# Performance work log

Measured on AMD Instinct MI355X. Metric: run time of the kernel, lower is better.

Reference implementation:

```python
import jax, jax.numpy as jnp
import numpy as np

N = 2048      # nodes: 8 sequences x 256 tokens
E = 524288    # edges: dense attention graph, 8 * 256^2
H = 8         # heads
DK = 64       # per-head dim


def setup_inputs() -> dict:
    key = jax.random.key(0)
    k1, k2, k3, k4, k5 = jax.random.split(key, 5)
    q = jax.random.normal(k1, (N, H, DK), dtype=jnp.float32)
    k = jax.random.normal(k2, (N, H, DK), dtype=jnp.float32)
    v = jax.random.normal(k3, (N, H, DK), dtype=jnp.float32)
    edge_src = jax.random.randint(k4, (E,), 0, N, dtype=jnp.int32)
    edge_dst = jax.random.randint(k5, (E,), 0, N, dtype=jnp.int32)
    return {"q": q, "k": k, "v": v, "edge_src": edge_src, "edge_dst": edge_dst}


def reference(q, k, v, edge_src, edge_dst):
    # src_dot_dst('k','q','score'): per-edge dot product over head dim -> [E, H]
    score = jnp.einsum('ehd,ehd->eh', k[edge_src], q[edge_dst])
    # scaled_exp('score', sqrt(d_k)): exp(clamp(score / sqrt(d_k), -10, 10))
    score = jnp.exp(jnp.clip(score / jnp.sqrt(jnp.float32(DK)), -10.0, 10.0))
    # send_and_recv: wv = sum_dst(v_src * score), z = sum_dst(score)
    wv = jax.ops.segment_sum(v[edge_src] * score[:, :, None], edge_dst, num_segments=N)  # [N, H, DK]
    z = jax.ops.segment_sum(score, edge_dst, num_segments=N)  # [N, H]
    # post_func normalization: attention output per node
    return wv / z[:, :, None]
```

## Files before the change

kernel.cpp:

```cpp
#include <hip/hip_runtime.h>

#define NNODES 2048
#define NHEAD 8
#define DKDIM 64

typedef unsigned int uint;
typedef unsigned short ushort;
typedef unsigned char uchar;
typedef __fp16 h2 __attribute__((ext_vector_type(2)));
typedef __fp16 h8 __attribute__((ext_vector_type(8)));
typedef float f4 __attribute__((ext_vector_type(4)));

#define KSCALE 0.18033688011112042f
#define CLAMP2 14.426950408889634f

__device__ __forceinline__ uint pk2(float a, float b) {
    union { h2 h; uint u; } x; x.h = __builtin_amdgcn_cvt_pkrtz(a, b); return x.u;
}

__global__ void conv_k(const float* __restrict__ k, uint4* __restrict__ kc,
                       uint4* __restrict__ A4) {
    int i = blockIdx.x * 256 + threadIdx.x;
    int dim8 = i & 7, node = (i >> 3) & 2047, h = i >> 14;
    const float* src = k + (size_t)node * 512 + h * 64 + dim8 * 8;
    float4 f0 = *(const float4*)src;
    float4 f1 = *(const float4*)(src + 4);
    uint4 o;
    o.x = pk2(f0.x * KSCALE, f0.y * KSCALE);
    o.y = pk2(f0.z * KSCALE, f0.w * KSCALE);
    o.z = pk2(f1.x * KSCALE, f1.y * KSCALE);
    o.w = pk2(f1.z * KSCALE, f1.w * KSCALE);
    kc[(h * 2048 + node) * 8 + dim8] = o;
    uint4 zz = {0u, 0u, 0u, 0u};
    A4[i] = zz;
    A4[i + 131072] = zz;
}

__global__ void conv_vT(const float* __restrict__ v, ushort* __restrict__ vt) {
    __shared__ float tile[64][65];
    int b = blockIdx.x;
    int h = b & 7, tn = b >> 3;
    int t = threadIdx.x;
    int nl = t >> 2, dq = (t & 3) * 16;
    const float* src = v + ((size_t)(tn * 64 + nl)) * 512 + h * 64 + dq;
#pragma unroll
    for (int i = 0; i < 4; ++i) {
        float4 f = *(const float4*)(src + i * 4);
        tile[nl][dq + i * 4 + 0] = f.x;
        tile[nl][dq + i * 4 + 1] = f.y;
        tile[nl][dq + i * 4 + 2] = f.z;
        tile[nl][dq + i * 4 + 3] = f.w;
    }
    __syncthreads();
    int dim = t >> 2, nq = (t & 3) * 16;
    uint wv[8];
#pragma unroll
    for (int i = 0; i < 8; ++i)
        wv[i] = pk2(tile[nq + 2 * i][dim], tile[nq + 2 * i + 1][dim]);
    char* base = (char*)vt + ((size_t)(h * 64 + dim) * 2048 + tn * 64) * 2;
    int nb0 = (t & 3) * 2;
    uint4 lo = { wv[0], wv[1], wv[2], wv[3] };
    uint4 hi = { wv[4], wv[5], wv[6], wv[7] };
    *(uint4*)(base + nb0 * 16) = lo;
    *(uint4*)(base + nb0 * 16 + 16) = hi;
}

__global__ void histA(const int* __restrict__ es, const int* __restrict__ ed,
                      uint* __restrict__ A32, int E) {
    int i = blockIdx.x * 256 + threadIdx.x;
    if (i < E) {
        uint idx = (uint)es[i] * 2048u + (uint)ed[i];
        atomicAdd(&A32[idx >> 2], 1u << ((idx & 3) * 8));
    }
}

__global__ void __launch_bounds__(512, 1) attn_kernel(
    const float* __restrict__ q, const ushort* __restrict__ kc, const ushort* __restrict__ vt,
    const uchar* __restrict__ A8, float* __restrict__ out) {
    __shared__ __align__(16) char LK[2][2][8192];
    __shared__ __align__(16) char LV[2][2][8192];
    __shared__ __align__(16) char LA[2][2][4096];
    __shared__ __align__(16) char LS[8][2304];

    int b = blockIdx.x;
    int h = b & 7;
    int dst0 = (b >> 3) * 64;
    int t = threadIdx.x;
    int w = t >> 6, half = w >> 2, wq = w & 3;
    int l = t & 63, c = l & 15, g = l >> 4;
    int ht = t & 255;

    const char* kH = (const char*)kc + (size_t)h * 262144;
    const char* vH = (const char*)vt + (size_t)h * 262144;

    h8 qf[2];
    {
        const float* qp = q + (size_t)(dst0 + wq * 16 + c) * 512 + h * 64 + g * 8;
#pragma unroll
        for (int ch = 0; ch < 2; ++ch) {
            float4 f0 = *(const float4*)(qp + ch * 32);
            float4 f1 = *(const float4*)(qp + ch * 32 + 4);
            union { uint u[4]; h8 v; } U;
            U.u[0] = pk2(f0.x, f0.y); U.u[1] = pk2(f0.z, f0.w);
            U.u[2] = pk2(f1.x, f1.y); U.u[3] = pk2(f1.z, f1.w);
            qf[ch] = U.v;
        }
    }

    f4 of[4];
#pragma unroll
    for (int i = 0; i < 4; ++i) of[i] = (f4){0.f, 0.f, 0.f, 0.f};
    float z = 0.f;

    int r0 = ht >> 3, b0 = ht & 7;
    int ar_ = ht >> 2, as_ = ht & 3;
    uint4 kr[2], vr[2], ar;
    int ts0 = half * 16;

#pragma unroll
    for (int j = 0; j < 2; ++j) {
        int row = r0 + j * 32;
        kr[j] = *(const uint4*)(kH + (size_t)(ts0 * 64 + row) * 128 + b0 * 16);
        vr[j] = *(const uint4*)(vH + (size_t)row * 4096 + ts0 * 128 + b0 * 16);
        *(uint4*)(LK[half][0] + row * 128 + b0 * 16) = kr[j];
        *(uint4*)(LV[half][0] + row * 128 + b0 * 16) = vr[j];
    }
    ar = *(const uint4*)(A8 + (size_t)(ts0 * 64 + ar_) * 2048 + dst0 + as_ * 16);
    *(uint4*)(LA[half][0] + ar_ * 64 + as_ * 16) = ar;
    __syncthreads();

    for (int it = 0; it < 16; ++it) {
        int cur = it & 1;
        int ts = ts0 + it;
        if (it < 15) {
#pragma unroll
            for (int j = 0; j < 2; ++j) {
                int row = r0 + j * 32;
                kr[j] = *(const uint4*)(kH + (size_t)((ts + 1) * 64 + row) * 128 + b0 * 16);
                vr[j] = *(const uint4*)(vH + (size_t)row * 4096 + (ts + 1) * 128 + b0 * 16);
            }
            ar = *(const uint4*)(A8 + (size_t)((ts + 1) * 64 + ar_) * 2048 + dst0 + as_ * 16);
        }

        f4 sacc[4];
#pragma unroll
        for (int i = 0; i < 4; ++i) sacc[i] = (f4){0.f, 0.f, 0.f, 0.f};
#pragma unroll
        for (int nt = 0; nt < 4; ++nt)
#pragma unroll
            for (int ch = 0; ch < 2; ++ch) {
                h8 kf = *(const h8*)(LK[half][cur] + (nt * 16 + c) * 128 + (ch * 4 + g) * 16);
                sacc[nt] = __builtin_amdgcn_mfma_f32_16x16x32_f16(kf, qf[ch], sacc[nt], 0, 0, 0);
            }

        char* Sw = LS[w];
        const uchar* Ac = (const uchar*)LA[half][cur];
#pragma unroll
        for (int nt = 0; nt < 4; ++nt)
#pragma unroll
            for (int r = 0; r < 4; ++r) {
                float sc = fminf(fmaxf(sacc[nt][r], -CLAMP2), CLAMP2);
                float m = (float)Ac[(nt * 16 + 4 * g + r) * 64 + wq * 16 + c];
                float e = exp2f(sc) * m;
                z += e;
                *(ushort*)(Sw + c * 144 + (nt * 16 + 4 * g + r) * 2) = (ushort)pk2(e, e);
            }
        asm volatile("" ::: "memory");

        h8 sf[2];
#pragma unroll
        for (int ch = 0; ch < 2; ++ch)
            sf[ch] = *(const h8*)(Sw + c * 144 + (ch * 32 + 8 * g) * 2);
#pragma unroll
        for (int nt = 0; nt < 4; ++nt)
#pragma unroll
            for (int ch = 0; ch < 2; ++ch) {
                h8 vf = *(const h8*)(LV[half][cur] + (nt * 16 + c) * 128 + (ch * 4 + g) * 16);
                of[nt] = __builtin_amdgcn_mfma_f32_16x16x32_f16(vf, sf[ch], of[nt], 0, 0, 0);
            }

        if (it < 15) {
            int nb = cur ^ 1;
#pragma unroll
            for (int j = 0; j < 2; ++j) {
                int row = r0 + j * 32;
                *(uint4*)(LK[half][nb] + row * 128 + b0 * 16) = kr[j];
                *(uint4*)(LV[half][nb] + row * 128 + b0 * 16) = vr[j];
            }
            *(uint4*)(LA[half][nb] + ar_ * 64 + as_ * 16) = ar;
        }
        __syncthreads();
    }

    z += __shfl_xor(z, 16);
    z += __shfl_xor(z, 32);

    float* CL = (float*)&LK[0][0][0];
    float* CLz = (float*)&LV[0][0][0];
    if (half == 1) {
#pragma unroll
        for (int nt = 0; nt < 4; ++nt)
#pragma unroll
            for (int r = 0; r < 4; ++r)
                CL[(wq * 16 + c) * 65 + nt * 16 + 4 * g + r] = of[nt][r];
        if (l < 16) CLz[wq * 16 + c] = z;
    }
    __syncthreads();
    if (half == 0) {
        float zt = 1.0f / (z + CLz[wq * 16 + c]);
#pragma unroll
        for (int nt = 0; nt < 4; ++nt)
#pragma unroll
            for (int r = 0; r < 4; ++r) {
                int idx = (wq * 16 + c) * 65 + nt * 16 + 4 * g + r;
                CL[idx] = (of[nt][r] + CL[idx]) * zt;
            }
    }
    __syncthreads();
#pragma unroll
    for (int j = 0; j < 8; ++j) {
        int i2 = w * 8 + j;
        out[(size_t)(dst0 + i2) * 512 + h * 64 + l] = CL[i2 * 65 + l];
    }
}


extern "C" void kernel_launch(void* const* d_in, const int* in_sizes, int n_in,
                              void* d_out, int out_size, void* d_ws, size_t ws_size,
                              hipStream_t stream) {
    const float* q = (const float*)d_in[0];
    const float* k = (const float*)d_in[1];
    const float* v = (const float*)d_in[2];
    const int* esrc = (const int*)d_in[3];
    const int* edst = (const int*)d_in[4];
    float* out = (float*)d_out;
    const int E = in_sizes[3];

    uchar* A8 = (uchar*)d_ws;
    ushort* kc = (ushort*)(A8 + (size_t)NNODES * NNODES);
    ushort* vt = kc + (size_t)NHEAD * NNODES * DKDIM;

    conv_k<<<512, 256, 0, stream>>>(k, (uint4*)kc, (uint4*)A8);
    conv_vT<<<256, 256, 0, stream>>>(v, vt);
    histA<<<(E + 255) / 256, 256, 0, stream>>>(esrc, edst, (uint*)A8, E);
    attn_kernel<<<256, 512, 0, stream>>>(q, kc, vt, A8, out);
}
```

Before: 69.28 us.

## Merge vT and histogram kernels, swizzle LDS, shuffle scores, transpose adjacency

Merges the V-transpose and edge-histogram prep kernels into one launch, which removes a kernel launch. Stores the adjacency count matrix as [dst][src] so each lane reads its four counts with a single 32-bit LDS load. Applies an XOR swizzle to the K/V LDS tiles to reduce bank conflicts, and passes the exp scores to the second MFMA through cross-lane shuffles instead of an LDS scratch round-trip. Adds s_setprio around the MFMA blocks; the shuffle-based transpose adds ALU and select work in exchange for less LDS traffic.

```diff
diff --git a/kernel.cpp b/kernel.cpp
--- a/kernel.cpp
+++ b/kernel.cpp
@@ -18,8 +18,8 @@
     union { h2 h; uint u; } x; x.h = __builtin_amdgcn_cvt_pkrtz(a, b); return x.u;
 }
 
-__global__ void conv_k(const float* __restrict__ k, uint4* __restrict__ kc,
-                       uint4* __restrict__ A4) {
+__global__ void prep1(const float* __restrict__ k, uint4* __restrict__ kc,
+                      uint4* __restrict__ A4) {
     int i = blockIdx.x * 256 + threadIdx.x;
     int dim8 = i & 7, node = (i >> 3) & 2047, h = i >> 14;
     const float* src = k + (size_t)node * 512 + h * 64 + dim8 * 8;
@@ -36,41 +36,42 @@
     A4[i + 131072] = zz;
 }
 
-__global__ void conv_vT(const float* __restrict__ v, ushort* __restrict__ vt) {
+__global__ void prep2(const float* __restrict__ v, ushort* __restrict__ vt,
+                      const int* __restrict__ es, const int* __restrict__ ed,
+                      uint* __restrict__ A32, int E) {
     __shared__ float tile[64][65];
     int b = blockIdx.x;
-    int h = b & 7, tn = b >> 3;
     int t = threadIdx.x;
-    int nl = t >> 2, dq = (t & 3) * 16;
-    const float* src = v + ((size_t)(tn * 64 + nl)) * 512 + h * 64 + dq;
-#pragma unroll
-    for (int i = 0; i < 4; ++i) {
-        float4 f = *(const float4*)(src + i * 4);
-        tile[nl][dq + i * 4 + 0] = f.x;
-        tile[nl][dq + i * 4 + 1] = f.y;
-        tile[nl][dq + i * 4 + 2] = f.z;
-        tile[nl][dq + i * 4 + 3] = f.w;
-    }
-    __syncthreads();
-    int dim = t >> 2, nq = (t & 3) * 16;
-    uint wv[8];
-#pragma unroll
-    for (int i = 0; i < 8; ++i)
-        wv[i] = pk2(tile[nq + 2 * i][dim], tile[nq + 2 * i + 1][dim]);
-    char* base = (char*)vt + ((size_t)(h * 64 + dim) * 2048 + tn * 64) * 2;
-    int nb0 = (t & 3) * 2;
-    uint4 lo = { wv[0], wv[1], wv[2], wv[3] };
-    uint4 hi = { wv[4], wv[5], wv[6], wv[7] };
-    *(uint4*)(base + nb0 * 16) = lo;
-    *(uint4*)(base + nb0 * 16 + 16) = hi;
-}
-
-__global__ void histA(const int* __restrict__ es, const int* __restrict__ ed,
-                      uint* __restrict__ A32, int E) {
-    int i = blockIdx.x * 256 + threadIdx.x;
-    if (i < E) {
-        uint idx = (uint)es[i] * 2048u + (uint)ed[i];
-        atomicAdd(&A32[idx >> 2], 1u << ((idx & 3) * 8));
+    if (b < 256) {
+        int h = b & 7, tn = b >> 3;
+        int nl = t >> 2, dq = (t & 3) * 16;
+        const float* src = v + ((size_t)(tn * 64 + nl)) * 512 + h * 64 + dq;
+#pragma unroll
+        for (int i = 0; i < 4; ++i) {
+            float4 f = *(const float4*)(src + i * 4);
+            tile[nl][dq + i * 4 + 0] = f.x;
+            tile[nl][dq + i * 4 + 1] = f.y;
+            tile[nl][dq + i * 4 + 2] = f.z;
+            tile[nl][dq + i * 4 + 3] = f.w;
+        }
+        __syncthreads();
+        int dim = t >> 2, nq = (t & 3) * 16;
+        uint wv[8];
+#pragma unroll
+        for (int i = 0; i < 8; ++i)
+            wv[i] = pk2(tile[nq + 2 * i][dim], tile[nq + 2 * i + 1][dim]);
+        char* base = (char*)vt + ((size_t)(b & 7) * 64 + dim) * 4096 + (b >> 3) * 128;
+        int nb0 = (t & 3) * 2;
+        uint4 lo = { wv[0], wv[1], wv[2], wv[3] };
+        uint4 hi = { wv[4], wv[5], wv[6], wv[7] };
+        *(uint4*)(base + nb0 * 16) = lo;
+        *(uint4*)(base + nb0 * 16 + 16) = hi;
+    } else {
+        int i = (b - 256) * 256 + t;
+        if (i < E) {
+            uint idx = (uint)ed[i] * 2048u + (uint)es[i];
+            atomicAdd(&A32[idx >> 2], 1u << ((idx & 3) * 8));
+        }
     }
 }
 
@@ -79,8 +80,7 @@
     const uchar* __restrict__ A8, float* __restrict__ out) {
     __shared__ __align__(16) char LK[2][2][8192];
     __shared__ __align__(16) char LV[2][2][8192];
-    __shared__ __align__(16) char LA[2][2][4096];
-    __shared__ __align__(16) char LS[8][2304];
+    __shared__ __align__(16) char LA[2][2][5120];
 
     int b = blockIdx.x;
     int h = b & 7;
@@ -114,20 +114,23 @@
 
     int r0 = ht >> 3, b0 = ht & 7;
     int ar_ = ht >> 2, as_ = ht & 3;
+    int ts0 = half * 16;
     uint4 kr[2], vr[2], ar;
-    int ts0 = half * 16;
 
 #pragma unroll
     for (int j = 0; j < 2; ++j) {
         int row = r0 + j * 32;
         kr[j] = *(const uint4*)(kH + (size_t)(ts0 * 64 + row) * 128 + b0 * 16);
         vr[j] = *(const uint4*)(vH + (size_t)row * 4096 + ts0 * 128 + b0 * 16);
-        *(uint4*)(LK[half][0] + row * 128 + b0 * 16) = kr[j];
-        *(uint4*)(LV[half][0] + row * 128 + b0 * 16) = vr[j];
-    }
-    ar = *(const uint4*)(A8 + (size_t)(ts0 * 64 + ar_) * 2048 + dst0 + as_ * 16);
-    *(uint4*)(LA[half][0] + ar_ * 64 + as_ * 16) = ar;
+        *(uint4*)(LK[half][0] + row * 128 + (b0 ^ (row & 7)) * 16) = kr[j];
+        *(uint4*)(LV[half][0] + row * 128 + (b0 ^ (row & 7)) * 16) = vr[j];
+    }
+    ar = *(const uint4*)(A8 + (size_t)(dst0 + ar_) * 2048 + ts0 * 64 + as_ * 16);
+    *(uint4*)(LA[half][0] + ar_ * 80 + as_ * 16) = ar;
     __syncthreads();
+
+    int sl = c + 32 * (g & 1);
+    bool hi = (g >> 1) != 0;
 
     for (int it = 0; it < 16; ++it) {
         int cur = it & 1;
@@ -139,55 +142,73 @@
                 kr[j] = *(const uint4*)(kH + (size_t)((ts + 1) * 64 + row) * 128 + b0 * 16);
                 vr[j] = *(const uint4*)(vH + (size_t)row * 4096 + (ts + 1) * 128 + b0 * 16);
             }
-            ar = *(const uint4*)(A8 + (size_t)((ts + 1) * 64 + ar_) * 2048 + dst0 + as_ * 16);
+            ar = *(const uint4*)(A8 + (size_t)(dst0 + ar_) * 2048 + (ts + 1) * 64 + as_ * 16);
         }
 
         f4 sacc[4];
 #pragma unroll
         for (int i = 0; i < 4; ++i) sacc[i] = (f4){0.f, 0.f, 0.f, 0.f};
+        __builtin_amdgcn_s_setprio(1);
 #pragma unroll
         for (int nt = 0; nt < 4; ++nt)
 #pragma unroll
             for (int ch = 0; ch < 2; ++ch) {
-                h8 kf = *(const h8*)(LK[half][cur] + (nt * 16 + c) * 128 + (ch * 4 + g) * 16);
+                h8 kf = *(const h8*)(LK[half][cur] + (nt * 16 + c) * 128 +
+                                     (((ch * 4 + g) ^ (c & 7)) * 16));
                 sacc[nt] = __builtin_amdgcn_mfma_f32_16x16x32_f16(kf, qf[ch], sacc[nt], 0, 0, 0);
             }
-
-        char* Sw = LS[w];
-        const uchar* Ac = (const uchar*)LA[half][cur];
-#pragma unroll
-        for (int nt = 0; nt < 4; ++nt)
+        __builtin_amdgcn_s_setprio(0);
+
+        uint pw[4][2];
+#pragma unroll
+        for (int nt = 0; nt < 4; ++nt) {
+            uint aw = *(const uint*)(LA[half][cur] + (wq * 16 + c) * 80 + nt * 16 + 4 * g);
+            float e[4];
 #pragma unroll
             for (int r = 0; r < 4; ++r) {
                 float sc = fminf(fmaxf(sacc[nt][r], -CLAMP2), CLAMP2);
-                float m = (float)Ac[(nt * 16 + 4 * g + r) * 64 + wq * 16 + c];
-                float e = exp2f(sc) * m;
-                z += e;
-                *(ushort*)(Sw + c * 144 + (nt * 16 + 4 * g + r) * 2) = (ushort)pk2(e, e);
-            }
-        asm volatile("" ::: "memory");
+                e[r] = exp2f(sc) * (float)((aw >> (8 * r)) & 255u);
+                z += e[r];
+            }
+            pw[nt][0] = pk2(e[0], e[1]);
+            pw[nt][1] = pk2(e[2], e[3]);
+        }
 
         h8 sf[2];
 #pragma unroll
-        for (int ch = 0; ch < 2; ++ch)
-            sf[ch] = *(const h8*)(Sw + c * 144 + (ch * 32 + 8 * g) * 2);
+        for (int ch = 0; ch < 2; ++ch) {
+            uint a0 = __shfl(pw[2 * ch][0], sl),      b0_ = __shfl(pw[2 * ch + 1][0], sl);
+            uint a1 = __shfl(pw[2 * ch][1], sl),      b1_ = __shfl(pw[2 * ch + 1][1], sl);
+            uint a2 = __shfl(pw[2 * ch][0], sl + 16), b2_ = __shfl(pw[2 * ch + 1][0], sl + 16);
+            uint a3 = __shfl(pw[2 * ch][1], sl + 16), b3_ = __shfl(pw[2 * ch + 1][1], sl + 16);
+            union { uint u[4]; h8 v; } S;
+            S.u[0] = hi ? b0_ : a0;
+            S.u[1] = hi ? b1_ : a1;
+            S.u[2] = hi ? b2_ : a2;
+            S.u[3] = hi ? b3_ : a3;
+            sf[ch] = S.v;
+        }
+
+        __builtin_amdgcn_s_setprio(1);
 #pragma unroll
         for (int nt = 0; nt < 4; ++nt)
 #pragma unroll
             for (int ch = 0; ch < 2; ++ch) {
-                h8 vf = *(const h8*)(LV[half][cur] + (nt * 16 + c) * 128 + (ch * 4 + g) * 16);
+                h8 vf = *(const h8*)(LV[half][cur] + (nt * 16 + c) * 128 +
+                                     (((ch * 4 + g) ^ (c & 7)) * 16));
                 of[nt] = __builtin_amdgcn_mfma_f32_16x16x32_f16(vf, sf[ch], of[nt], 0, 0, 0);
             }
+        __builtin_amdgcn_s_setprio(0);
 
         if (it < 15) {
             int nb = cur ^ 1;
 #pragma unroll
             for (int j = 0; j < 2; ++j) {
                 int row = r0 + j * 32;
-                *(uint4*)(LK[half][nb] + row * 128 + b0 * 16) = kr[j];
-                *(uint4*)(LV[half][nb] + row * 128 + b0 * 16) = vr[j];
-            }
-            *(uint4*)(LA[half][nb] + ar_ * 64 + as_ * 16) = ar;
+                *(uint4*)(LK[half][nb] + row * 128 + (b0 ^ (row & 7)) * 16) = kr[j];
+                *(uint4*)(LV[half][nb] + row * 128 + (b0 ^ (row & 7)) * 16) = vr[j];
+            }
+            *(uint4*)(LA[half][nb] + ar_ * 80 + as_ * 16) = ar;
         }
         __syncthreads();
     }
@@ -240,8 +261,7 @@
     ushort* kc = (ushort*)(A8 + (size_t)NNODES * NNODES);
     ushort* vt = kc + (size_t)NHEAD * NNODES * DKDIM;
 
-    conv_k<<<512, 256, 0, stream>>>(k, (uint4*)kc, (uint4*)A8);
-    conv_vT<<<256, 256, 0, stream>>>(v, vt);
-    histA<<<(E + 255) / 256, 256, 0, stream>>>(esrc, edst, (uint*)A8, E);
+    prep1<<<512, 256, 0, stream>>>(k, (uint4*)kc, (uint4*)A8);
+    prep2<<<2304, 256, 0, stream>>>(v, vt, esrc, edst, (uint*)A8, E);
     attn_kernel<<<256, 512, 0, stream>>>(q, kc, vt, A8, out);
 }
```

Measured after the change: 64.66 us. 6.7% less time.
